# Performance work log

Measured on AMD Instinct MI355X. Metric: run time of the kernel, lower is better.

The kernel has to match this reference:

```python
import jax, jax.numpy as jnp
import numpy as np

WINDOW = 21
PATCH = 1
H_PARAM = 0.1
EPS = 1e-10


def _box_sum(x, w):
    # Sum over a w x w sliding window (VALID), per (batch, channel).
    return jax.lax.reduce_window(x, 0.0, jax.lax.add,
                                 (1, 1, w, w), (1, 1, 1, 1), 'VALID')


def setup_inputs() -> dict:
    key = jax.random.key(0)
    noisy = jax.random.uniform(key, (8, 3, 512, 512), dtype=jnp.float32)
    return {"noisy": noisy}


def reference(noisy) -> jnp.ndarray:
    # Faithful vectorization of the per-pixel loop for patch_size=1.
    # For each pixel p=(i,j):
    #   window = padded[i:i+W, j:j+W]; center = noisy[i,j]
    #   dists  = mean((window - center)^2)
    #   weights = exp(-dists / h^2)            # shape (B, C)
    #   patch  = window[0, 0] = padded[i, j]   # top-left of window (half_patch=0)
    #   out[:, c, i, j] = sum_b weights[b,c] * patch[b,c]   (sum over BATCH)
    #   wsum[:, c, i, j] = sum_b weights[b,c]
    # out = clamp(out / (wsum + 1e-10), 0, 1)
    h2 = H_PARAM * H_PARAM
    W = WINDOW
    pad = W // 2
    B, C, Hh, Ww = noisy.shape
    padded = jnp.pad(noisy, ((0, 0), (0, 0), (pad, pad), (pad, pad)), mode='reflect')

    # mean((window - center)^2) = (S2 - 2*center*S1 + W^2*center^2) / W^2
    s1 = _box_sum(padded, W)                  # (B, C, H, W)
    s2 = _box_sum(padded * padded, W)
    n_win = jnp.asarray(W * W, dtype=noisy.dtype)
    dists = (s2 - 2.0 * noisy * s1 + n_win * noisy * noisy) / n_win

    weights = jnp.exp(-dists / h2)            # (B, C, H, W)
    patch = padded[:, :, :Hh, :Ww]            # top-left pixel of each window

    num = jnp.sum(weights * patch, axis=0, keepdims=True)   # (1, C, H, W)
    den = jnp.sum(weights, axis=0, keepdims=True)
    out = num / (den + EPS)
    out = jnp.broadcast_to(out, noisy.shape)  # loop assigns same row to all b
    return jnp.clip(out, 0.0, 1.0)
```

## Files before the change

### kernel.cpp

```cpp
#include <hip/hip_runtime.h>

#define B 8
#define CCH 3
#define HH 512
#define WW 512
#define WIN 21
#define PAD 10
#define TSX 32
#define TSY 16
#define PTX 52
#define PTY 36
#define TROW 56
#define HROW 38

__global__ __launch_bounds__(256) void nlm_fused_kernel(const float* __restrict__ noisy,
                                                        float* __restrict__ out) {
    __shared__ float  tile[PTY][TROW];
    __shared__ float2 hs_t[TSX][HROW];

    const int tid = threadIdx.x;
    const int tx  = tid & 31;
    const int ty0 = (tid >> 5) * 2;

    const int x0 = blockIdx.x * TSX;
    const int y0 = blockIdx.y * TSY;
    const int ch = blockIdx.z;

    float num0 = 0.f, num1 = 0.f, den0 = 0.f, den1 = 0.f;

    for (int b = 0; b < B; ++b) {
        const float* src = noisy + (size_t)(b * CCH + ch) * (HH * WW);

        for (int s = tid; s < PTY * 13; s += 256) {
            int r  = s / 13;
            int c4 = s - r * 13;
            int gy = y0 + r - PAD;
            gy = (gy < 0) ? -gy : ((gy >= HH) ? (2 * (HH - 1) - gy) : gy);
            int gxs = x0 + (c4 << 2) - PAD;
            float4 v;
            if (gxs >= 0 && gxs <= WW - 4) {
                v = *(const float4*)(src + gy * WW + gxs);
            } else {
                float tmp[4];
                #pragma unroll
                for (int t = 0; t < 4; ++t) {
                    int gx = gxs + t;
                    gx = (gx < 0) ? -gx : ((gx >= WW) ? (2 * (WW - 1) - gx) : gx);
                    tmp[t] = src[gy * WW + gx];
                }
                v = make_float4(tmp[0], tmp[1], tmp[2], tmp[3]);
            }
            *(float4*)&tile[r][c4 << 2] = v;
        }
        __syncthreads();

        for (int u = tid; u < PTY * 8; u += 256) {
            int r   = u >> 3;
            int cx0 = (u & 7) << 2;
            float v[24];
            #pragma unroll
            for (int q = 0; q < 6; ++q)
                *(float4*)&v[q * 4] = *(const float4*)&tile[r][cx0 + q * 4];
            float s1 = 0.f, s2 = 0.f;
            #pragma unroll
            for (int k = 0; k < WIN; ++k) { s1 += v[k]; s2 += v[k] * v[k]; }
            hs_t[cx0][r] = make_float2(s1, s2);
            #pragma unroll
            for (int j = 1; j < 4; ++j) {
                float vo = v[j - 1], vn = v[j + WIN - 1];
                s1 += vn - vo;
                s2 += vn * vn - vo * vo;
                hs_t[cx0 + j][r] = make_float2(s1, s2);
            }
        }
        __syncthreads();

        float4 q0 = *(const float4*)&hs_t[tx][ty0];
        float vs1 = q0.x + q0.z, vs2 = q0.y + q0.w;
        #pragma unroll
        for (int k = 1; k < 10; ++k) {
            float4 q = *(const float4*)&hs_t[tx][ty0 + 2 * k];
            vs1 += q.x + q.z;
            vs2 += q.y + q.w;
        }
        float4 q10 = *(const float4*)&hs_t[tx][ty0 + 20];
        vs1 += q10.x;
        vs2 += q10.y;
        {
            float a = tile[ty0 + PAD][tx + PAD];
            float p = tile[ty0][tx];
            float dd = vs2 - 2.f * a * vs1 + 441.f * a * a;
            float w = __expf(dd * (-100.f / 441.f));
            num0 += w * p;
            den0 += w;
        }
        vs1 += q10.z - q0.x;
        vs2 += q10.w - q0.y;
        {
            float a = tile[ty0 + 1 + PAD][tx + PAD];
            float p = tile[ty0 + 1][tx];
            float dd = vs2 - 2.f * a * vs1 + 441.f * a * a;
            float w = __expf(dd * (-100.f / 441.f));
            num1 += w * p;
            den1 += w;
        }
        __syncthreads();
    }

    {
        int y = y0 + ty0;
        int x = x0 + tx;
        float v0 = num0 / (den0 + 1e-10f);
        v0 = v0 < 0.f ? 0.f : (v0 > 1.f ? 1.f : v0);
        float v1 = num1 / (den1 + 1e-10f);
        v1 = v1 < 0.f ? 0.f : (v1 > 1.f ? 1.f : v1);
        #pragma unroll
        for (int b = 0; b < B; ++b) {
            size_t base = ((size_t)(b * CCH + ch) * HH + y) * WW + x;
            out[base] = v0;
            out[base + WW] = v1;
        }
    }
}

extern "C" void kernel_launch(void* const* d_in, const int* in_sizes, int n_in,
                              void* d_out, int out_size, void* d_ws, size_t ws_size,
                              hipStream_t stream) {
    const float* noisy = (const float*)d_in[0];
    float* out = (float*)d_out;
    dim3 grid(WW / TSX, HH / TSY, CCH);
    nlm_fused_kernel<<<grid, dim3(256), 0, stream>>>(noisy, out);
}
```

Measured before the change: 103.3 us.

## Parallelize over batch with atomic accumulation and separate finalize kernel

The per-block loop over the batch is removed. Batch now goes into the grid z dimension, and each block writes its weighted num and den into a float2 workspace with atomicAdd. A second kernel divides, clamps and broadcasts the result to all batch slices. Tiles grow to 32x32 with 4 rows per thread, which cuts halo overhead and raises grid parallelism from 3 to 24 planes. In exchange it adds a memset, atomic traffic, an extra launch, and non-deterministic float summation order.

```diff
diff --git a/kernel.cpp b/kernel.cpp
--- a/kernel.cpp
+++ b/kernel.cpp
@@ -7,119 +7,138 @@
 #define WIN 21
 #define PAD 10
 #define TSX 32
-#define TSY 16
-#define PTX 52
-#define PTY 36
+#define TSY 32
+#define PTY 52
 #define TROW 56
-#define HROW 38
+#define HROW 54
 
-__global__ __launch_bounds__(256) void nlm_fused_kernel(const float* __restrict__ noisy,
-                                                        float* __restrict__ out) {
+__global__ __launch_bounds__(256) void nlm_accum_kernel(const float* __restrict__ noisy,
+                                                        float2* __restrict__ ws) {
     __shared__ float  tile[PTY][TROW];
     __shared__ float2 hs_t[TSX][HROW];
 
     const int tid = threadIdx.x;
-    const int tx  = tid & 31;
-    const int ty0 = (tid >> 5) * 2;
-
     const int x0 = blockIdx.x * TSX;
     const int y0 = blockIdx.y * TSY;
-    const int ch = blockIdx.z;
+    const int ch = blockIdx.z % CCH;
+    const int b  = blockIdx.z / CCH;
 
-    float num0 = 0.f, num1 = 0.f, den0 = 0.f, den1 = 0.f;
+    const float* src = noisy + (size_t)(b * CCH + ch) * (HH * WW);
 
-    for (int b = 0; b < B; ++b) {
-        const float* src = noisy + (size_t)(b * CCH + ch) * (HH * WW);
+    for (int s = tid; s < PTY * 13; s += 256) {
+        int r  = s / 13;
+        int c4 = s - r * 13;
+        int gy = y0 + r - PAD;
+        gy = (gy < 0) ? -gy : ((gy >= HH) ? (2 * (HH - 1) - gy) : gy);
+        int gxs = x0 + (c4 << 2) - PAD;
+        float4 v;
+        if (gxs >= 0 && gxs <= WW - 4) {
+            v = *(const float4*)(src + gy * WW + gxs);
+        } else {
+            float tmp[4];
+            #pragma unroll
+            for (int t = 0; t < 4; ++t) {
+                int gx = gxs + t;
+                gx = (gx < 0) ? -gx : ((gx >= WW) ? (2 * (WW - 1) - gx) : gx);
+                tmp[t] = src[gy * WW + gx];
+            }
+            v = make_float4(tmp[0], tmp[1], tmp[2], tmp[3]);
+        }
+        *(float4*)&tile[r][c4 << 2] = v;
+    }
+    __syncthreads();
 
-        for (int s = tid; s < PTY * 13; s += 256) {
-            int r  = s / 13;
-            int c4 = s - r * 13;
-            int gy = y0 + r - PAD;
-            gy = (gy < 0) ? -gy : ((gy >= HH) ? (2 * (HH - 1) - gy) : gy);
-            int gxs = x0 + (c4 << 2) - PAD;
-            float4 v;
-            if (gxs >= 0 && gxs <= WW - 4) {
-                v = *(const float4*)(src + gy * WW + gxs);
-            } else {
-                float tmp[4];
-                #pragma unroll
-                for (int t = 0; t < 4; ++t) {
-                    int gx = gxs + t;
-                    gx = (gx < 0) ? -gx : ((gx >= WW) ? (2 * (WW - 1) - gx) : gx);
-                    tmp[t] = src[gy * WW + gx];
-                }
-                v = make_float4(tmp[0], tmp[1], tmp[2], tmp[3]);
-            }
-            *(float4*)&tile[r][c4 << 2] = v;
+    if (tid < PTY * 4) {
+        int r   = tid >> 2;
+        int cx0 = (tid & 3) << 3;
+        float v[28];
+        #pragma unroll
+        for (int q = 0; q < 7; ++q)
+            *(float4*)&v[q * 4] = *(const float4*)&tile[r][cx0 + q * 4];
+        float s1 = 0.f, s2 = 0.f;
+        #pragma unroll
+        for (int k = 0; k < WIN; ++k) { s1 += v[k]; s2 = fmaf(v[k], v[k], s2); }
+        hs_t[cx0][r] = make_float2(s1, s2);
+        #pragma unroll
+        for (int j = 1; j < 8; ++j) {
+            float vo = v[j - 1], vn = v[j + WIN - 1];
+            s1 += vn - vo;
+            s2 += vn * vn - vo * vo;
+            hs_t[cx0 + j][r] = make_float2(s1, s2);
         }
-        __syncthreads();
+    }
+    __syncthreads();
 
-        for (int u = tid; u < PTY * 8; u += 256) {
-            int r   = u >> 3;
-            int cx0 = (u & 7) << 2;
-            float v[24];
-            #pragma unroll
-            for (int q = 0; q < 6; ++q)
-                *(float4*)&v[q * 4] = *(const float4*)&tile[r][cx0 + q * 4];
-            float s1 = 0.f, s2 = 0.f;
-            #pragma unroll
-            for (int k = 0; k < WIN; ++k) { s1 += v[k]; s2 += v[k] * v[k]; }
-            hs_t[cx0][r] = make_float2(s1, s2);
-            #pragma unroll
-            for (int j = 1; j < 4; ++j) {
-                float vo = v[j - 1], vn = v[j + WIN - 1];
-                s1 += vn - vo;
-                s2 += vn * vn - vo * vo;
-                hs_t[cx0 + j][r] = make_float2(s1, s2);
-            }
-        }
-        __syncthreads();
+    const int tx  = tid & 31;
+    const int ty0 = (tid >> 5) << 2;
 
-        float4 q0 = *(const float4*)&hs_t[tx][ty0];
-        float vs1 = q0.x + q0.z, vs2 = q0.y + q0.w;
-        #pragma unroll
-        for (int k = 1; k < 10; ++k) {
-            float4 q = *(const float4*)&hs_t[tx][ty0 + 2 * k];
-            vs1 += q.x + q.z;
-            vs2 += q.y + q.w;
-        }
-        float4 q10 = *(const float4*)&hs_t[tx][ty0 + 20];
-        vs1 += q10.x;
-        vs2 += q10.y;
-        {
-            float a = tile[ty0 + PAD][tx + PAD];
-            float p = tile[ty0][tx];
-            float dd = vs2 - 2.f * a * vs1 + 441.f * a * a;
-            float w = __expf(dd * (-100.f / 441.f));
-            num0 += w * p;
-            den0 += w;
-        }
-        vs1 += q10.z - q0.x;
-        vs2 += q10.w - q0.y;
-        {
-            float a = tile[ty0 + 1 + PAD][tx + PAD];
-            float p = tile[ty0 + 1][tx];
-            float dd = vs2 - 2.f * a * vs1 + 441.f * a * a;
-            float w = __expf(dd * (-100.f / 441.f));
-            num1 += w * p;
-            den1 += w;
-        }
-        __syncthreads();
+    float4 q0 = *(const float4*)&hs_t[tx][ty0];
+    float4 q1 = *(const float4*)&hs_t[tx][ty0 + 2];
+    float vs1 = q0.x + q0.z + q1.x + q1.z;
+    float vs2 = q0.y + q0.w + q1.y + q1.w;
+    #pragma unroll
+    for (int k = 2; k < 10; ++k) {
+        float4 q = *(const float4*)&hs_t[tx][ty0 + 2 * k];
+        vs1 += q.x + q.z;
+        vs2 += q.y + q.w;
+    }
+    float4 q10 = *(const float4*)&hs_t[tx][ty0 + 20];
+    float4 q11 = *(const float4*)&hs_t[tx][ty0 + 22];
+    vs1 += q10.x;
+    vs2 += q10.y;
+
+    float wv[4], wp[4];
+    {
+        float a = tile[ty0 + PAD][tx + PAD];
+        float p = tile[ty0][tx];
+        float dd = vs2 - 2.f * a * vs1 + 441.f * a * a;
+        float w = __expf(dd * (-100.f / 441.f));
+        wv[0] = w; wp[0] = w * p;
+    }
+    vs1 += q10.z - q0.x;  vs2 += q10.w - q0.y;
+    {
+        float a = tile[ty0 + 1 + PAD][tx + PAD];
+        float p = tile[ty0 + 1][tx];
+        float dd = vs2 - 2.f * a * vs1 + 441.f * a * a;
+        float w = __expf(dd * (-100.f / 441.f));
+        wv[1] = w; wp[1] = w * p;
+    }
+    vs1 += q11.x - q0.z;  vs2 += q11.y - q0.w;
+    {
+        float a = tile[ty0 + 2 + PAD][tx + PAD];
+        float p = tile[ty0 + 2][tx];
+        float dd = vs2 - 2.f * a * vs1 + 441.f * a * a;
+        float w = __expf(dd * (-100.f / 441.f));
+        wv[2] = w; wp[2] = w * p;
+    }
+    vs1 += q11.z - q1.x;  vs2 += q11.w - q1.y;
+    {
+        float a = tile[ty0 + 3 + PAD][tx + PAD];
+        float p = tile[ty0 + 3][tx];
+        float dd = vs2 - 2.f * a * vs1 + 441.f * a * a;
+        float w = __expf(dd * (-100.f / 441.f));
+        wv[3] = w; wp[3] = w * p;
     }
 
-    {
-        int y = y0 + ty0;
+    #pragma unroll
+    for (int i = 0; i < 4; ++i) {
+        int y = y0 + ty0 + i;
         int x = x0 + tx;
-        float v0 = num0 / (den0 + 1e-10f);
-        v0 = v0 < 0.f ? 0.f : (v0 > 1.f ? 1.f : v0);
-        float v1 = num1 / (den1 + 1e-10f);
-        v1 = v1 < 0.f ? 0.f : (v1 > 1.f ? 1.f : v1);
-        #pragma unroll
-        for (int b = 0; b < B; ++b) {
-            size_t base = ((size_t)(b * CCH + ch) * HH + y) * WW + x;
-            out[base] = v0;
-            out[base + WW] = v1;
-        }
+        float2* dst = ws + ((size_t)(ch * HH + y) * WW + x);
+        atomicAdd(&dst->x, wp[i]);
+        atomicAdd(&dst->y, wv[i]);
+    }
+}
+
+__global__ __launch_bounds__(256) void nlm_finalize_kernel(const float2* __restrict__ ws,
+                                                           float* __restrict__ out) {
+    int i = blockIdx.x * 256 + threadIdx.x;
+    float2 nd = ws[i];
+    float v = nd.x / (nd.y + 1e-10f);
+    v = v < 0.f ? 0.f : (v > 1.f ? 1.f : v);
+    #pragma unroll
+    for (int b = 0; b < B; ++b) {
+        out[(size_t)b * (CCH * HH * WW) + i] = v;
     }
 }
 
@@ -128,6 +147,13 @@
                               hipStream_t stream) {
     const float* noisy = (const float*)d_in[0];
     float* out = (float*)d_out;
-    dim3 grid(WW / TSX, HH / TSY, CCH);
-    nlm_fused_kernel<<<grid, dim3(256), 0, stream>>>(noisy, out);
+    float2* ws = (float2*)d_ws;
+
+    hipMemsetAsync(d_ws, 0, (size_t)CCH * HH * WW * sizeof(float2), stream);
+
+    dim3 grid1(WW / TSX, HH / TSY, CCH * B);
+    nlm_accum_kernel<<<grid1, dim3(256), 0, stream>>>(noisy, ws);
+
+    dim3 grid2((CCH * HH * WW) / 256);
+    nlm_finalize_kernel<<<grid2, dim3(256), 0, stream>>>(ws, out);
 }
```

Measured after the change: 155.4 us. +50.4%, slower.
